# Kernel tuning notes

Measured on AMD Instinct MI355X. Metric: run time of the kernel, lower is better.

Reference implementation:

```python
import jax, jax.numpy as jnp
import numpy as np

B, L, D, NHEADS, P = 64, 256, 768, 8, 3
VOCAB, DEP, NLAYERS = 30522, 45, 2
LAM = 0.5


def _forward(src_mask, aspect_mask, lex, attention_mask,
             tok_emb, seg_emb, pool_w, pool_b, ln_a, ln_b,
             dep_emb, fc1_w, fc1_b, fc2_w, fc2_b,
             aq_w, aq_b, ak_w, ak_b, lq_w, lq_b, lk_w, lk_b, root_w,
             gcn_w, gcn_b, fc3_w, fc3_b, cls_w, cls_b, vlin_w,
             text_bert_indices, bert_segments_ids, ori_tag, head):
    b, l = text_bert_indices.shape
    d = tok_emb.shape[1]
    dk = d // NHEADS
    NEG = jnp.float32(-1e30)
    # stand-in BERT encoder: token + segment embeddings, tanh pooler on [CLS]
    seq = tok_emb[text_bert_indices] + seg_emb[bert_segments_ids]
    pooled = jnp.tanh(seq[:, 0] @ pool_w + pool_b)
    # torch LayerNorm variant: unbiased std (ddof=1)
    mean = seq.mean(-1, keepdims=True)
    std = jnp.std(seq, axis=-1, keepdims=True, ddof=1)
    gcn_in = ln_a * (seq - mean) / (std + 1e-6) + ln_b
    # in-place fmask[:,0]=1 mutates src_mask storage in torch -> effective mask
    sm = src_mask.at[:, 0].set(1.0)
    # dependency-tag score -> per-token softmax -> scatter into [L,L] adjacency
    dep_h = jax.nn.relu(dep_emb[ori_tag] @ fc1_w + fc1_b)
    dep_s = (dep_h @ fc2_w + fc2_b)[..., 0]                      # [B,L]
    dep_feat = jax.nn.softmax(dep_s * sm + (1.0 - sm) * NEG, axis=1)
    to_idx = jnp.arange(1, l)
    fro = head[:, :l - 1]                                        # [B,L-1]
    b_idx = jnp.arange(b)[:, None]
    vals = dep_feat[:, :l - 1]
    dep_adj = jnp.ones((b, l, l), jnp.float32)
    dep_adj = dep_adj.at[b_idx, fro, to_idx[None, :]].set(vals)
    dep_adj = dep_adj.at[b_idx, to_idx[None, :], fro].set(vals)
    # multi-head attention-as-adjacency (returns softmax weights only)
    q = (gcn_in @ aq_w + aq_b).reshape(b, l, NHEADS, dk).transpose(0, 2, 1, 3)
    k = (gcn_in @ ak_w + ak_b).reshape(b, l, NHEADS, dk).transpose(0, 2, 1, 3)
    scores = jnp.einsum('bhqd,bhkd->bhqk', q, k) / (jnp.sqrt(jnp.float32(dk)) + 1e-9)
    scores = jnp.where(sm[:, None, None, :] == 0, jnp.float32(-1e9), scores)
    adj_ag = jax.nn.softmax(scores, axis=-1).mean(axis=1)        # [B,L,L]
    eye = jnp.eye(l, dtype=jnp.float32)
    adj_ag = (adj_ag * (1.0 - eye) + eye) * sm[:, :, None]
    # structured latent attention (stand-in for missing StructuredAtt):
    # masked bilinear attention biased by dep_adj + root attention loss
    q2 = gcn_in @ lq_w + lq_b
    k2 = gcn_in @ lk_w + lk_b
    lat = jnp.einsum('bqd,bkd->bqk', q2, k2) / jnp.sqrt(jnp.float32(d))
    lat = lat + dep_adj + (1.0 - sm)[:, None, :] * (-10000.0)
    adj_latent = jax.nn.softmax(lat, axis=-1)
    root_p = jax.nn.softmax((gcn_in @ root_w)[..., 0] * sm + (1.0 - sm) * NEG, axis=1)
    loss_root = -jnp.mean(jnp.log(jnp.sum(root_p * aspect_mask, axis=1) + 1e-9))
    adj_latent = (adj_latent * (1.0 - eye) + eye) * sm[:, :, None]
    # gated dual-adjacency GCN layers
    H_l = gcn_in
    I_sem = gcn_in
    for layer in range(gcn_w.shape[0]):
        g_l = jax.nn.sigmoid(H_l)
        I_sem = (adj_ag @ H_l) @ gcn_w[layer] + gcn_b[layer]
        I_lat = (adj_latent @ H_l) @ gcn_w[layer] + gcn_b[layer]
        g = jax.nn.sigmoid(I_lat)
        lam_g = LAM * g
        I_com = (1.0 - lam_g) * I_sem + lam_g * I_lat
        H_out = jax.nn.relu(I_com @ fc3_w + fc3_b)
        H_l = g_l * H_out + (1.0 - g_l) * H_l
    # readout
    asp_wn = aspect_mask.sum(axis=1, keepdims=True)              # [B,1]
    m3 = sm[:, :, None]
    h_l = H_l * m3
    h_sem = I_sem * m3
    beta = jnp.einsum('bqd,bkd->bqk', h_l, h_sem) / 1000.0
    attn_o = jax.nn.softmax(beta.sum(axis=1, keepdims=True), axis=2)  # [B,1,L]
    outputs = (attn_o @ I_sem)[:, 0]                             # [B,D]
    sem_pool = (I_sem * aspect_mask[:, :, None]).sum(axis=1) / (asp_wn + 1e-9)
    final = jnp.concatenate([outputs, sem_pool, pooled], axis=-1)  # [B,3D]
    logits = final @ cls_w + cls_b
    e = (H_l @ vlin_w)[..., 0]
    lw = jax.nn.softmax(e, axis=1) * 50.0
    lw = lw * sm.at[:, 0].set(0.0)
    lexicon_loss = jnp.mean((lw - lex) ** 2)
    return logits, loss_root, lexicon_loss


def setup_inputs() -> dict:
    key = jax.random.key(0)
    ks = jax.random.split(key, 24)
    s = 0.02
    n = lambda i, shape: jax.random.normal(ks[i], shape, dtype=jnp.float32) * s
    inp = {}
    inp['text_bert_indices'] = jax.random.randint(ks[0], (B, L), 0, VOCAB, dtype=jnp.int32)
    inp['bert_segments_ids'] = jnp.zeros((B, L), jnp.int32)
    inp['attention_mask'] = jnp.ones((B, L), jnp.float32)
    inp['src_mask'] = jnp.ones((B, L), jnp.float32)
    inp['aspect_mask'] = jax.random.randint(ks[1], (B, L), 0, 2).astype(jnp.float32)
    inp['lex'] = jax.random.uniform(ks[2], (B, L), dtype=jnp.float32)
    inp['ori_tag'] = jax.random.randint(ks[3], (B, L), 0, DEP, dtype=jnp.int32)
    inp['head'] = jax.random.randint(ks[4], (B, L), 0, L, dtype=jnp.int32)
    inp['tok_emb'] = n(5, (VOCAB, D)); inp['seg_emb'] = n(6, (2, D))
    inp['pool_w'] = n(7, (D, D)); inp['pool_b'] = jnp.zeros((D,), jnp.float32)
    inp['ln_a'] = jnp.ones((D,), jnp.float32); inp['ln_b'] = jnp.zeros((D,), jnp.float32)
    inp['dep_emb'] = n(8, (DEP, 300))
    inp['fc1_w'] = n(9, (300, 256)); inp['fc1_b'] = jnp.zeros((256,), jnp.float32)
    inp['fc2_w'] = n(10, (256, 1)); inp['fc2_b'] = jnp.zeros((1,), jnp.float32)
    inp['aq_w'] = n(11, (D, D)); inp['aq_b'] = jnp.zeros((D,), jnp.float32)
    inp['ak_w'] = n(12, (D, D)); inp['ak_b'] = jnp.zeros((D,), jnp.float32)
    inp['lq_w'] = n(13, (D, D)); inp['lq_b'] = jnp.zeros((D,), jnp.float32)
    inp['lk_w'] = n(14, (D, D)); inp['lk_b'] = jnp.zeros((D,), jnp.float32)
    inp['root_w'] = n(15, (D, 1))
    inp['gcn_w'] = n(16, (NLAYERS, D, D)); inp['gcn_b'] = jnp.zeros((NLAYERS, D), jnp.float32)
    inp['fc3_w'] = n(17, (D, D)); inp['fc3_b'] = jnp.zeros((D,), jnp.float32)
    inp['cls_w'] = n(18, (3 * D, P)); inp['cls_b'] = jnp.zeros((P,), jnp.float32)
    inp['vlin_w'] = n(19, (D, 1))
    return inp


def reference(text_bert_indices, bert_segments_ids, attention_mask, src_mask, aspect_mask, lex,
              ori_tag, head, tok_emb, seg_emb, pool_w, pool_b, ln_a, ln_b, dep_emb,
              fc1_w, fc1_b, fc2_w, fc2_b, aq_w, aq_b, ak_w, ak_b, lq_w, lq_b, lk_w, lk_b,
              root_w, gcn_w, gcn_b, fc3_w, fc3_b, cls_w, cls_b, vlin_w):
    return _forward(src_mask, aspect_mask, lex, attention_mask,
                    tok_emb, seg_emb, pool_w, pool_b, ln_a, ln_b,
                    dep_emb, fc1_w, fc1_b, fc2_w, fc2_b,
                    aq_w, aq_b, ak_w, ak_b, lq_w, lq_b, lk_w, lk_b, root_w,
                    gcn_w, gcn_b, fc3_w, fc3_b, cls_w, cls_b, vlin_w,
                    text_bert_indices, bert_segments_ids, ori_tag, head)
```

## Files before the change

### kernel.cpp

```cpp
#include <hip/hip_runtime.h>
#include <hip/hip_bf16.h>
#include <math.h>

#define DI __device__ __forceinline__

constexpr int cB = 64, cL = 256, cD = 768;
constexpr long BLD = (long)cB * cL * cD;
constexpr long BLL = (long)cB * cL * cL;
constexpr long cLL = (long)cL * cL;
constexpr long cLD = (long)cL * cD;

typedef __attribute__((ext_vector_type(8))) short b8;
typedef __attribute__((ext_vector_type(4))) float f4;

#define GLDS(g, l)                                                    \
  __builtin_amdgcn_global_load_lds(                                   \
      (const __attribute__((address_space(1))) void*)(g),             \
      (__attribute__((address_space(3))) void*)(l), 16, 0, 0)

DI float wsum(float v) {
#pragma unroll
  for (int o = 32; o > 0; o >>= 1) v += __shfl_down(v, o, 64);
  return v;
}
DI float wsum_all(float v) {
#pragma unroll
  for (int m = 32; m > 0; m >>= 1) v += __shfl_xor(v, m, 64);
  return v;
}
DI float wmax_all(float v) {
#pragma unroll
  for (int m = 32; m > 0; m >>= 1) v = fmaxf(v, __shfl_xor(v, m, 64));
  return v;
}
DI float wmaxr(float v) {
#pragma unroll
  for (int o = 32; o > 0; o >>= 1) v = fmaxf(v, __shfl_down(v, o, 64));
  return v;
}
DI float blockSum(float v) {
  __shared__ float sh[4];
  v = wsum(v);
  __syncthreads();
  if ((threadIdx.x & 63) == 0) sh[threadIdx.x >> 6] = v;
  __syncthreads();
  return sh[0] + sh[1] + sh[2] + sh[3];
}
DI float blockMax(float v) {
  __shared__ float sh[4];
  v = wmaxr(v);
  __syncthreads();
  if ((threadIdx.x & 63) == 0) sh[threadIdx.x >> 6] = v;
  __syncthreads();
  return fmaxf(fmaxf(sh[0], sh[1]), fmaxf(sh[2], sh[3]));
}
DI float sigf(float x) { return 1.f / (1.f + expf(-x)); }

template <int OBF, int RELU, int BIAS, int EPI>
__global__ __launch_bounds__(256, 2) void bgemm(
    const __hip_bfloat16* __restrict__ A, const __hip_bfloat16* __restrict__ BT,
    void* __restrict__ Cv, const float* __restrict__ bias,
    float* __restrict__ auxf, __hip_bfloat16* __restrict__ auxb,
    int K, int lda, int ldb, int ldc,
    int zshift, int zmask, long sA1, long sA2, long sB1, long sB2, long sC,
    int czdiv) {
  __shared__ __hip_bfloat16 Asp[128 * 32];
  __shared__ __hip_bfloat16 Bsp[128 * 32];
  int z = blockIdx.z;
  A += (long)(z >> zshift) * sA1 + (long)(z & zmask) * sA2;
  BT += (long)(z >> zshift) * sB1 + (long)(z & zmask) * sB2;
  int tid = threadIdx.x;
  int lane = tid & 63, w = tid >> 6;
  int wr = w >> 1, wc = w & 1;
  int l16 = lane & 15, q = lane >> 4;
  int m0 = blockIdx.y << 7, n0 = blockIdx.x << 7;

  int fm = tid >> 2, fq = tid & 3;
  const __hip_bfloat16* Ap0 = A + (long)(m0 + fm) * lda + fq * 8;
  const __hip_bfloat16* Ap1 = A + (long)(m0 + fm + 64) * lda + fq * 8;
  const __hip_bfloat16* Bp0 = BT + (long)(n0 + fm) * ldb + fq * 8;
  const __hip_bfloat16* Bp1 = BT + (long)(n0 + fm + 64) * ldb + fq * 8;
  char* Aw0 = (char*)Asp + (w << 10);
  char* Aw1 = (char*)Asp + 4096 + (w << 10);
  char* Bw0 = (char*)Bsp + (w << 10);
  char* Bw1 = (char*)Bsp + 4096 + (w << 10);

  f4 acc[4][4];
#pragma unroll
  for (int i = 0; i < 4; i++)
#pragma unroll
    for (int j = 0; j < 4; j++) acc[i][j] = (f4){0.f, 0.f, 0.f, 0.f};

  for (int k0 = 0; k0 < K; k0 += 32) {
    GLDS(Ap0 + k0, Aw0);
    GLDS(Ap1 + k0, Aw1);
    GLDS(Bp0 + k0, Bw0);
    GLDS(Bp1 + k0, Bw1);
    __syncthreads();
    b8 af[4], bf[4];
#pragma unroll
    for (int i = 0; i < 4; i++)
      af[i] = *(const b8*)&Asp[(wr * 64 + i * 16 + l16) * 32 + q * 8];
#pragma unroll
    for (int j = 0; j < 4; j++)
      bf[j] = *(const b8*)&Bsp[(wc * 64 + j * 16 + l16) * 32 + q * 8];
#pragma unroll
    for (int i = 0; i < 4; i++)
#pragma unroll
      for (int j = 0; j < 4; j++)
        acc[i][j] = __builtin_amdgcn_mfma_f32_16x16x32_bf16(af[i], bf[j], acc[i][j], 0, 0, 0);
    __syncthreads();
  }
  if (EPI == 4) {
#pragma unroll
    for (int j = 0; j < 4; j++) {
      int n = n0 + wc * 64 + j * 16 + l16;
#pragma unroll
      for (int i = 0; i < 4; i++) {
        int m = m0 + wr * 64 + i * 16 + (q << 2);
        __hip_bfloat16 t4[4];
#pragma unroll
        for (int r = 0; r < 4; r++) t4[r] = __float2bfloat16(acc[i][j][r]);
        long bidx = (long)(m >> 8) * sC + (long)n * cL + (m & 255);
        *(uint2*)&((__hip_bfloat16*)Cv)[bidx] = *(uint2*)t4;
      }
    }
    return;
  }
  long cz = (long)(z >> czdiv) * sC;
#pragma unroll
  for (int j = 0; j < 4; j++) {
    int n = n0 + wc * 64 + j * 16 + l16;
    float bv = BIAS ? bias[n] : 0.f;
#pragma unroll
    for (int i = 0; i < 4; i++) {
#pragma unroll
      for (int r = 0; r < 4; r++) {
        int m = m0 + wr * 64 + i * 16 + q * 4 + r;
        long idx = cz + (long)m * ldc + n;
        float v = acc[i][j][r] + bv;
        if (EPI == 0) {
          if (RELU) v = fmaxf(v, 0.f);
          if (OBF)
            ((__hip_bfloat16*)Cv)[idx] = __float2bfloat16(v);
          else
            ((float*)Cv)[idx] = v;
        } else if (EPI == 3) {
          atomicAdd(&((float*)Cv)[idx], v);
        } else {
          v = fmaxf(v, 0.f);
          float h = auxf[idx];
          float g = sigf(h);
          float o = h + g * (v - h);
          auxf[idx] = o;
          auxb[idx] = __float2bfloat16(o);
        }
      }
    }
  }
}

__global__ __launch_bounds__(256, 2) void bgemm_dual(
    const __hip_bfloat16* __restrict__ A1g, const __hip_bfloat16* __restrict__ A2g,
    const __hip_bfloat16* __restrict__ BTg, float* __restrict__ IsemF,
    __hip_bfloat16* __restrict__ Icb, const float* __restrict__ bias,
    int write_isem) {
  __shared__ __hip_bfloat16 A1sp[128 * 32];
  __shared__ __hip_bfloat16 A2sp[128 * 32];
  __shared__ __hip_bfloat16 Bsp[128 * 32];
  int z = blockIdx.z;
  const __hip_bfloat16* A1 = A1g + (long)z * cLL;
  const __hip_bfloat16* A2 = A2g + (long)z * cLL;
  const __hip_bfloat16* BT = BTg + (long)z * cLD;
  int tid = threadIdx.x;
  int lane = tid & 63, w = tid >> 6;
  int wr = w >> 1, wc = w & 1;
  int l16 = lane & 15, q = lane >> 4;
  int m0 = blockIdx.y << 7, n0 = blockIdx.x << 7;

  int fm = tid >> 2, fq = tid & 3;
  const __hip_bfloat16* A1p0 = A1 + (long)(m0 + fm) * cL + fq * 8;
  const __hip_bfloat16* A1p1 = A1p0 + 64L * cL;
  const __hip_bfloat16* A2p0 = A2 + (long)(m0 + fm) * cL + fq * 8;
  const __hip_bfloat16* A2p1 = A2p0 + 64L * cL;
  const __hip_bfloat16* Bp0 = BT + (long)(n0 + fm) * cL + fq * 8;
  const __hip_bfloat16* Bp1 = Bp0 + 64L * cL;
  char* w10 = (char*)A1sp + (w << 10);
  char* w11 = (char*)A1sp + 4096 + (w << 10);
  char* w20 = (char*)A2sp + (w << 10);
  char* w21 = (char*)A2sp + 4096 + (w << 10);
  char* wb0 = (char*)Bsp + (w << 10);
  char* wb1 = (char*)Bsp + 4096 + (w << 10);

  f4 ac1[4][4], ac2[4][4];
#pragma unroll
  for (int i = 0; i < 4; i++)
#pragma unroll
    for (int j = 0; j < 4; j++) {
      ac1[i][j] = (f4){0.f, 0.f, 0.f, 0.f};
      ac2[i][j] = (f4){0.f, 0.f, 0.f, 0.f};
    }

  for (int k0 = 0; k0 < cL; k0 += 32) {
    GLDS(A1p0 + k0, w10);
    GLDS(A1p1 + k0, w11);
    GLDS(A2p0 + k0, w20);
    GLDS(A2p1 + k0, w21);
    GLDS(Bp0 + k0, wb0);
    GLDS(Bp1 + k0, wb1);
    __syncthreads();
    b8 a1f[4], a2f[4], bf[4];
#pragma unroll
    for (int i = 0; i < 4; i++) {
      a1f[i] = *(const b8*)&A1sp[(wr * 64 + i * 16 + l16) * 32 + q * 8];
      a2f[i] = *(const b8*)&A2sp[(wr * 64 + i * 16 + l16) * 32 + q * 8];
    }
#pragma unroll
    for (int j = 0; j < 4; j++)
      bf[j] = *(const b8*)&Bsp[(wc * 64 + j * 16 + l16) * 32 + q * 8];
#pragma unroll
    for (int i = 0; i < 4; i++)
#pragma unroll
      for (int j = 0; j < 4; j++) {
        ac1[i][j] = __builtin_amdgcn_mfma_f32_16x16x32_bf16(a1f[i], bf[j], ac1[i][j], 0, 0, 0);
        ac2[i][j] = __builtin_amdgcn_mfma_f32_16x16x32_bf16(a2f[i], bf[j], ac2[i][j], 0, 0, 0);
      }
    __syncthreads();
  }
  long cz = (long)z * cLD;
#pragma unroll
  for (int j = 0; j < 4; j++) {
    int n = n0 + wc * 64 + j * 16 + l16;
    float bv = bias[n];
#pragma unroll
    for (int i = 0; i < 4; i++) {
#pragma unroll
      for (int r = 0; r < 4; r++) {
        int m = m0 + wr * 64 + i * 16 + q * 4 + r;
        long idx = cz + (long)m * cD + n;
        float is = ac1[i][j][r] + bv;
        float il = ac2[i][j][r] + bv;
        float g = 0.5f * sigf(il);
        Icb[idx] = __float2bfloat16(is + g * (il - is));
        if (write_isem) IsemF[idx] = is;
      }
    }
  }
}

__global__ void k_wconv7(const float* __restrict__ s0, const float* __restrict__ s1,
                         const float* __restrict__ s2, const float* __restrict__ s3,
                         const float* __restrict__ s4, const float* __restrict__ s5,
                         const float* __restrict__ s6, __hip_bfloat16* __restrict__ dst) {
  const float* srcs[7] = {s0, s1, s2, s3, s4, s5, s6};
  const float* src = srcs[blockIdx.z];
  __hip_bfloat16* d = dst + (long)blockIdx.z * cD * cD;
  __shared__ float t[32][33];
  int k0 = blockIdx.x * 32, n0 = blockIdx.y * 32;
  int tx = threadIdx.x, ty = threadIdx.y;
#pragma unroll
  for (int i = 0; i < 32; i += 8) t[ty + i][tx] = src[(long)(k0 + ty + i) * cD + n0 + tx];
  __syncthreads();
#pragma unroll
  for (int i = 0; i < 32; i += 8)
    d[(long)(n0 + ty + i) * cD + k0 + tx] = __float2bfloat16(t[tx][ty + i]);
}

__global__ __launch_bounds__(256) void k_gcnin(
    const int* __restrict__ tbi, const int* __restrict__ bsi,
    const float* __restrict__ tok, const float* __restrict__ seg,
    const float* __restrict__ ln_a, const float* __restrict__ ln_b,
    const float* __restrict__ root_w,
    float* __restrict__ gcn_in, __hip_bfloat16* __restrict__ gib,
    float* __restrict__ x64, float* __restrict__ e1) {
  long bl = blockIdx.x;
  int t = tbi[bl], s = bsi[bl];
  const float* tr = tok + (long)t * cD;
  const float* sr = seg + (long)s * cD;
  float x[3];
  float ls = 0.f;
#pragma unroll
  for (int i = 0; i < 3; i++) {
    int d = threadIdx.x + (i << 8);
    x[i] = tr[d] + sr[d];
    ls += x[i];
  }
  if ((bl & 255) == 0) {
#pragma unroll
    for (int i = 0; i < 3; i++) x64[(bl >> 8) * cD + threadIdx.x + (i << 8)] = x[i];
  }
  float mean = blockSum(ls) * (1.f / 768.f);
  float lv = 0.f;
#pragma unroll
  for (int i = 0; i < 3; i++) { float c = x[i] - mean; lv += c * c; }
  float var = blockSum(lv) * (1.f / 767.f);
  float inv = 1.f / (sqrtf(var) + 1e-6f);
  float rdot = 0.f;
#pragma unroll
  for (int i = 0; i < 3; i++) {
    int d = threadIdx.x + (i << 8);
    float v = ln_a[d] * (x[i] - mean) * inv + ln_b[d];
    gcn_in[bl * cD + d] = v;
    gib[bl * cD + d] = __float2bfloat16(v);
    rdot += v * root_w[d];
  }
  float tot = blockSum(rdot);
  if (threadIdx.x == 0) e1[bl] = tot;
}

__global__ __launch_bounds__(256) void k_pool1(
    const float* __restrict__ x64, const float* __restrict__ pw,
    float* __restrict__ pacc) {
  __shared__ float pws[48][256];
  __shared__ float xs[16][48];
  int i0 = blockIdx.x * 48, j0 = blockIdx.y * 256, b0 = blockIdx.z * 16;
  for (int r = 0; r < 48; r++) pws[r][threadIdx.x] = pw[(long)(i0 + r) * cD + j0 + threadIdx.x];
  for (int idx = threadIdx.x; idx < 16 * 48; idx += 256)
    xs[idx / 48][idx % 48] = x64[(long)(b0 + idx / 48) * cD + i0 + idx % 48];
  __syncthreads();
  int j = threadIdx.x;
  for (int b = 0; b < 16; b++) {
    float acc = 0.f;
#pragma unroll 8
    for (int i = 0; i < 48; i++) acc += xs[b][i] * pws[i][j];
    atomicAdd(&pacc[(long)(b0 + b) * cD + j0 + j], acc);
  }
}
__global__ __launch_bounds__(256) void k_pool2(
    const float* __restrict__ pacc, const float* __restrict__ pb,
    float* __restrict__ pooled) {
  int b = blockIdx.x;
#pragma unroll
  for (int c = 0; c < 3; c++) {
    int j = (c << 8) + threadIdx.x;
    pooled[(long)b * cD + j] = tanhf(pacc[(long)b * cD + j] + pb[j]);
  }
}

__global__ __launch_bounds__(256) void k_s45(
    const float* __restrict__ dep_emb, const float* __restrict__ fc1w,
    const float* __restrict__ fc1b, const float* __restrict__ fc2w,
    const float* __restrict__ fc2b, float* __restrict__ s45) {
  int t = blockIdx.x;
  __shared__ float e[300];
  for (int i = threadIdx.x; i < 300; i += 256) e[i] = dep_emb[t * 300 + i];
  __syncthreads();
  int j = threadIdx.x;
  float h = fc1b[j];
  for (int i = 0; i < 300; i++) h += e[i] * fc1w[i * 256 + j];
  h = fmaxf(h, 0.f);
  float tot = blockSum(h * fc2w[j]);
  if (threadIdx.x == 0) s45[t] = tot + fc2b[0];
}

__global__ __launch_bounds__(256) void k_depfeat(
    const int* __restrict__ ori, const float* __restrict__ src_mask,
    const float* __restrict__ s45, float* __restrict__ dep_feat) {
  int b = blockIdx.x, l = threadIdx.x;
  float smv = (l == 0) ? 1.f : src_mask[b * cL + l];
  float sc = s45[ori[b * cL + l]] * smv + (1.f - smv) * (-1e30f);
  float mx = blockMax(sc);
  float ex = expf(sc - mx);
  float sum = blockSum(ex);
  dep_feat[b * cL + l] = ex / sum;
}

__global__ void k_bcat(const float* __restrict__ a, const float* __restrict__ b,
                       const float* __restrict__ c, const float* __restrict__ d,
                       float* __restrict__ o) {
  int i = blockIdx.x * 256 + threadIdx.x;
  float v = (i < 768) ? a[i] : (i < 1536) ? b[i - 768] : (i < 2304) ? c[i - 1536] : d[i - 2304];
  o[i] = v;
}

__global__ __launch_bounds__(256) void k_adjag_sm(
    const __hip_bfloat16* __restrict__ scores, const float* __restrict__ src_mask,
    __hip_bfloat16* __restrict__ adjag) {
  int b = blockIdx.x >> 8, i = blockIdx.x & 255;
  int tid = threadIdx.x, wave = tid >> 6, lane = tid & 63;
  __shared__ float accs[4][256];
  const float scale = 1.f / (sqrtf(96.f) + 1e-9f);
  float smj[4], acc[4];
#pragma unroll
  for (int c = 0; c < 4; c++) {
    int j = c * 64 + lane;
    smj[c] = (j == 0) ? 1.f : src_mask[b * cL + j];
    acc[c] = 0.f;
  }
  for (int hh = 0; hh < 2; hh++) {
    int h = wave * 2 + hh;
    const __hip_bfloat16* row = scores + (((long)(b * 8 + h)) * cL + i) * cL;
    float s[4], m = -1e30f;
#pragma unroll
    for (int c = 0; c < 4; c++) {
      s[c] = (smj[c] == 0.f) ? -1e9f : __bfloat162float(row[c * 64 + lane]) * scale;
      m = fmaxf(m, s[c]);
    }
    m = wmax_all(m);
    float es = 0.f;
#pragma unroll
    for (int c = 0; c < 4; c++) { s[c] = expf(s[c] - m); es += s[c]; }
    es = wsum_all(es);
    float inv = 1.f / es;
#pragma unroll
    for (int c = 0; c < 4; c++) acc[c] += s[c] * inv;
  }
#pragma unroll
  for (int c = 0; c < 4; c++) accs[wave][c * 64 + lane] = acc[c];
  __syncthreads();
  int j = tid;
  float tot = accs[0][j] + accs[1][j] + accs[2][j] + accs[3][j];
  float smi = (i == 0) ? 1.f : src_mask[b * cL + i];
  float v = (j == i) ? 1.f : tot * 0.125f;
  adjag[((long)b * cL + i) * cL + j] = __float2bfloat16(v * smi);
}

__global__ __launch_bounds__(256) void k_adjlat_sm(
    const float* __restrict__ latsc, const int* __restrict__ head,
    const float* __restrict__ df, const float* __restrict__ src_mask,
    __hip_bfloat16* __restrict__ adjlat) {
  int b = blockIdx.x >> 8, i = blockIdx.x & 255;
  int j = threadIdx.x;
  float smj = (j == 0) ? 1.f : src_mask[b * cL + j];
  float dep = 1.f;
  if (j >= 1 && head[b * cL + j - 1] == i) dep = df[b * cL + j - 1];
  if (i >= 1 && j == head[b * cL + i - 1]) dep = df[b * cL + i - 1];
  float s = latsc[((long)b * cL + i) * cL + j] * (1.f / sqrtf(768.f)) +
            dep + (1.f - smj) * (-10000.f);
  float mx = blockMax(s);
  float ex = expf(s - mx);
  float sum = blockSum(ex);
  float p = ex / sum;
  float smi = (i == 0) ? 1.f : src_mask[b * cL + i];
  adjlat[((long)b * cL + i) * cL + j] = __float2bfloat16(((j == i) ? 1.f : p) * smi);
}

__global__ __launch_bounds__(256) void k_rowdot(
    const float* __restrict__ X, const float* __restrict__ w, long wstride,
    float* __restrict__ e) {
  int r = blockIdx.x * 4 + (threadIdx.x >> 6);
  int lane = threadIdx.x & 63;
  const float4* row = (const float4*)(X + (long)r * cD);
  const float4* wp = (const float4*)(w + (long)(r >> 8) * wstride);
  float s = 0.f;
#pragma unroll
  for (int c = 0; c < 3; c++) {
    int idx = c * 64 + lane;
    float4 a = row[idx], b = wp[idx];
    s += a.x * b.x + a.y * b.y + a.z * b.z + a.w * b.w;
  }
  s = wsum(s);
  if (lane == 0) e[r] = s;
}

__global__ __launch_bounds__(256) void k_root2(
    const float* __restrict__ e1, const float* __restrict__ src_mask,
    const float* __restrict__ aspect_mask, float* __restrict__ out_loss) {
  int b = blockIdx.x, l = threadIdx.x;
  float r = e1[b * cL + l];
  float smv = (l == 0) ? 1.f : src_mask[b * cL + l];
  float sc = r * smv + (1.f - smv) * (-1e30f);
  float mx = blockMax(sc);
  float ex = expf(sc - mx);
  float sum = blockSum(ex);
  float p = ex / sum;
  float tot = blockSum(p * aspect_mask[b * cL + l]);
  if (l == 0) atomicAdd(out_loss, -logf(tot + 1e-9f) * (1.f / 64.f));
}

__global__ __launch_bounds__(256) void k_lex2(
    const float* __restrict__ e2, const float* __restrict__ src_mask,
    const float* __restrict__ lex, float* __restrict__ out_loss) {
  int b = blockIdx.x, l = threadIdx.x;
  float e = e2[b * cL + l];
  float mx = blockMax(e);
  float ex = expf(e - mx);
  float sum = blockSum(ex);
  float mult = (l == 0) ? 0.f : src_mask[b * cL + l];
  float lw = ex / sum * 50.f * mult;
  float d2 = lw - lex[b * cL + l];
  float tot = blockSum(d2 * d2);
  if (l == 0) atomicAdd(out_loss, tot * (1.f / (64.f * 256.f)));
}

__global__ __launch_bounds__(256) void k_hl(
    const float* __restrict__ H, const float* __restrict__ src_mask,
    float* __restrict__ hlsum) {
// ... 67 lines not shown
  const int* tbi = (const int*)d_in[0];
  const int* bsi = (const int*)d_in[1];
  const float* src_mask = (const float*)d_in[3];
  const float* aspect_mask = (const float*)d_in[4];
  const float* lex = (const float*)d_in[5];
  const int* ori = (const int*)d_in[6];
  const int* head = (const int*)d_in[7];
  const float* tok_emb = (const float*)d_in[8];
  const float* seg_emb = (const float*)d_in[9];
  const float* pool_w = (const float*)d_in[10];
  const float* pool_b = (const float*)d_in[11];
  const float* ln_a = (const float*)d_in[12];
  const float* ln_b = (const float*)d_in[13];
  const float* dep_emb = (const float*)d_in[14];
  const float* fc1_w = (const float*)d_in[15];
  const float* fc1_b = (const float*)d_in[16];
  const float* fc2_w = (const float*)d_in[17];
  const float* fc2_b = (const float*)d_in[18];
  const float* aq_w = (const float*)d_in[19];
  const float* aq_b = (const float*)d_in[20];
  const float* ak_w = (const float*)d_in[21];
  const float* ak_b = (const float*)d_in[22];
  const float* lq_w = (const float*)d_in[23];
  const float* lq_b = (const float*)d_in[24];
  const float* lk_w = (const float*)d_in[25];
  const float* lk_b = (const float*)d_in[26];
  const float* root_w = (const float*)d_in[27];
  const float* gcn_w = (const float*)d_in[28];
  const float* gcn_b = (const float*)d_in[29];
  const float* fc3_w = (const float*)d_in[30];
  const float* fc3_b = (const float*)d_in[31];
  const float* cls_w = (const float*)d_in[32];
  const float* cls_b = (const float*)d_in[33];
  const float* vlin_w = (const float*)d_in[34];

  float* out = (float*)d_out;
  float* ws = (float*)d_ws;
  float* gcnH = ws;
  float* Isem = gcnH + BLD;
  float* depfeat = Isem + BLD;
  float* s45 = depfeat + cB * cL;
  float* pooled = s45 + 64;
  float* x64 = pooled + cB * cD;
  float* hlsum = x64 + cB * cD;
  float* outputs = hlsum + cB * cD;
  float* sempool = outputs + cB * cD;
  float* pacc = sempool + cB * cD;
  float* e1 = pacc + cB * cD;
  float* e2 = e1 + cB * cL;
  float* sraw = e2 + cB * cL;
  float* wgt = sraw + cB * cL;
  float* asum = wgt + cB * cL;
  float* catb = asum + 64;
  float* latsc = Isem;
  __hip_bfloat16* gib = (__hip_bfloat16*)(catb + 3072);
  __hip_bfloat16* qkb = gib + BLD;
  __hip_bfloat16* scores = qkb + 4 * BLD;
  __hip_bfloat16* adjag_b = scores + 8 * BLL;
  __hip_bfloat16* adjlat_b = adjag_b + BLL;
  __hip_bfloat16* wbt = adjlat_b + BLL;
  __hip_bfloat16* HWbT = qkb + BLD;
  __hip_bfloat16* Icb = qkb + 2 * BLD;

  hipMemsetAsync((char*)d_out + 192 * sizeof(float), 0, 2 * sizeof(float), stream);
  hipMemsetAsync(hlsum, 0, 4 * cB * cD * sizeof(float), stream);
  hipMemsetAsync(latsc, 0, BLL * sizeof(float), stream);

  k_gcnin<<<cB * cL, 256, 0, stream>>>(tbi, bsi, tok_emb, seg_emb, ln_a, ln_b,
                                       root_w, gcnH, gib, x64, e1);
  k_s45<<<45, 256, 0, stream>>>(dep_emb, fc1_w, fc1_b, fc2_w, fc2_b, s45);
  k_depfeat<<<cB, 256, 0, stream>>>(ori, src_mask, s45, depfeat);
  k_pool1<<<dim3(16, 3, 4), 256, 0, stream>>>(x64, pool_w, pacc);
  k_pool2<<<cB, 256, 0, stream>>>(pacc, pool_b, pooled);
  k_bcat<<<12, 256, 0, stream>>>(aq_b, ak_b, lq_b, lk_b, catb);
  k_wconv7<<<dim3(24, 24, 7), dim3(32, 8), 0, stream>>>(
      aq_w, ak_w, lq_w, lk_w, gcn_w, gcn_w + (long)cD * cD, fc3_w, wbt);

  const long DD = (long)cD * cD;
  const long LD = cLD, LL = cLL;
  const long LP = (long)cL * 3072;

  bgemm<1, 0, 1, 0><<<dim3(24, 128, 1), 256, 0, stream>>>(
      gib, wbt, qkb, catb, nullptr, nullptr, cD, cD, cD, 3072,
      0, 0, 0, 0, 0, 0, 0, 0);

  bgemm<1, 0, 0, 0><<<dim3(2, 2, cB * 8), 256, 0, stream>>>(
      qkb, qkb + 768, scores, nullptr, nullptr, nullptr,
      96, 3072, 3072, cL, 3, 7, LP, 96, LP, 96, LL, 0);
  k_adjag_sm<<<cB * cL, 256, 0, stream>>>(scores, src_mask, adjag_b);

  bgemm<0, 0, 0, 3><<<dim3(2, 2, cB * 2), 256, 0, stream>>>(
      qkb + 1536, qkb + 2304, latsc, nullptr, nullptr, nullptr,
      384, 3072, 3072, cL, 1, 1, LP, 384, LP, 384, LL, 1);
  k_adjlat_sm<<<cB * cL, 256, 0, stream>>>(latsc, head, depfeat, src_mask, adjlat_b);

  k_root2<<<cB, 256, 0, stream>>>(e1, src_mask, aspect_mask, out + 192);

  for (int layer = 0; layer < 2; layer++) {
    const float* bb = gcn_b + (long)layer * cD;
    bgemm<1, 0, 0, 4><<<dim3(6, 128, 1), 256, 0, stream>>>(
        gib, wbt + (4 + layer) * DD, HWbT, nullptr, nullptr, nullptr,
        cD, cD, cD, cD, 0, 0, 0, 0, 0, 0, LD, 0);
    bgemm_dual<<<dim3(6, 2, cB), 256, 0, stream>>>(
        adjag_b, adjlat_b, HWbT, Isem, Icb, bb, layer == 1 ? 1 : 0);
    bgemm<0, 1, 1, 2><<<dim3(6, 128, 1), 256, 0, stream>>>(
        Icb, wbt + 6 * DD, nullptr, fc3_b, gcnH, gib,
        cD, cD, cD, cD, 0, 0, 0, 0, 0, 0, 0, 0);
  }

  k_hl<<<dim3(8, 3, cB), 256, 0, stream>>>(gcnH, src_mask, hlsum);
  k_rowdot<<<cB * cL / 4, 256, 0, stream>>>(Isem, hlsum, cD, sraw);
  k_attnw<<<cB, 256, 0, stream>>>(sraw, src_mask, aspect_mask, wgt, asum);
  k_wsum<<<dim3(8, 3, cB), 256, 0, stream>>>(Isem, wgt, aspect_mask, outputs, sempool);
  k_logits<<<cB, 256, 0, stream>>>(outputs, sempool, pooled, asum, cls_w, cls_b, out);
  k_rowdot<<<cB * cL / 4, 256, 0, stream>>>(gcnH, vlin_w, 0, e2);
  k_lex2<<<cB, 256, 0, stream>>>(e2, src_mask, lex, out + 193);
}
```

Before: 889.8 us.

## Double-buffer LDS tiles in bgemm and bgemm_dual to overlap loads with MFMA

Both GEMM kernels now keep two LDS buffers per operand. Each iteration issues the global-to-LDS loads for the next K tile before running MFMAs on the current one, and keeps a single barrier per iteration. The goal is to hide global load latency behind compute. The cost is double the LDS use, which may lower occupancy, and there is a correctness risk because global_load_lds completion is not explicitly waited on before the barrier.

```diff
diff --git a/kernel.cpp b/kernel.cpp
--- a/kernel.cpp
+++ b/kernel.cpp
@@ -64,8 +64,8 @@
     int K, int lda, int ldb, int ldc,
     int zshift, int zmask, long sA1, long sA2, long sB1, long sB2, long sC,
     int czdiv) {
-  __shared__ __hip_bfloat16 Asp[128 * 32];
-  __shared__ __hip_bfloat16 Bsp[128 * 32];
+  __shared__ __hip_bfloat16 Asp[2][128 * 32];
+  __shared__ __hip_bfloat16 Bsp[2][128 * 32];
   int z = blockIdx.z;
   A += (long)(z >> zshift) * sA1 + (long)(z & zmask) * sA2;
   BT += (long)(z >> zshift) * sB1 + (long)(z & zmask) * sB2;
@@ -91,25 +91,37 @@
 #pragma unroll
     for (int j = 0; j < 4; j++) acc[i][j] = (f4){0.f, 0.f, 0.f, 0.f};
 
+  GLDS(Ap0, Aw0);
+  GLDS(Ap1, Aw1);
+  GLDS(Bp0, Bw0);
+  GLDS(Bp1, Bw1);
+  __syncthreads();
+  int cur = 0;
   for (int k0 = 0; k0 < K; k0 += 32) {
-    GLDS(Ap0 + k0, Aw0);
-    GLDS(Ap1 + k0, Aw1);
-    GLDS(Bp0 + k0, Bw0);
-    GLDS(Bp1 + k0, Bw1);
-    __syncthreads();
+    int k1 = k0 + 32;
+    if (k1 < K) {
+      int nb = (cur ^ 1) * 8192;
+      GLDS(Ap0 + k1, Aw0 + nb);
+      GLDS(Ap1 + k1, Aw1 + nb);
+      GLDS(Bp0 + k1, Bw0 + nb);
+      GLDS(Bp1 + k1, Bw1 + nb);
+    }
+    const __hip_bfloat16* As = Asp[cur];
+    const __hip_bfloat16* Bs = Bsp[cur];
     b8 af[4], bf[4];
 #pragma unroll
     for (int i = 0; i < 4; i++)
-      af[i] = *(const b8*)&Asp[(wr * 64 + i * 16 + l16) * 32 + q * 8];
+      af[i] = *(const b8*)&As[(wr * 64 + i * 16 + l16) * 32 + q * 8];
 #pragma unroll
     for (int j = 0; j < 4; j++)
-      bf[j] = *(const b8*)&Bsp[(wc * 64 + j * 16 + l16) * 32 + q * 8];
+      bf[j] = *(const b8*)&Bs[(wc * 64 + j * 16 + l16) * 32 + q * 8];
 #pragma unroll
     for (int i = 0; i < 4; i++)
 #pragma unroll
       for (int j = 0; j < 4; j++)
         acc[i][j] = __builtin_amdgcn_mfma_f32_16x16x32_bf16(af[i], bf[j], acc[i][j], 0, 0, 0);
     __syncthreads();
+    cur ^= 1;
   }
   if (EPI == 4) {
 #pragma unroll
@@ -165,9 +177,9 @@
     const __hip_bfloat16* __restrict__ BTg, float* __restrict__ IsemF,
     __hip_bfloat16* __restrict__ Icb, const float* __restrict__ bias,
     int write_isem) {
-  __shared__ __hip_bfloat16 A1sp[128 * 32];
-  __shared__ __hip_bfloat16 A2sp[128 * 32];
-  __shared__ __hip_bfloat16 Bsp[128 * 32];
+  __shared__ __hip_bfloat16 A1sp[2][128 * 32];
+  __shared__ __hip_bfloat16 A2sp[2][128 * 32];
+  __shared__ __hip_bfloat16 Bsp[2][128 * 32];
   int z = blockIdx.z;
   const __hip_bfloat16* A1 = A1g + (long)z * cLL;
   const __hip_bfloat16* A2 = A2g + (long)z * cLL;
@@ -201,23 +213,37 @@
       ac2[i][j] = (f4){0.f, 0.f, 0.f, 0.f};
     }
 
+  GLDS(A1p0, w10);
+  GLDS(A1p1, w11);
+  GLDS(A2p0, w20);
+  GLDS(A2p1, w21);
+  GLDS(Bp0, wb0);
+  GLDS(Bp1, wb1);
+  __syncthreads();
+  int cur = 0;
   for (int k0 = 0; k0 < cL; k0 += 32) {
-    GLDS(A1p0 + k0, w10);
-    GLDS(A1p1 + k0, w11);
-    GLDS(A2p0 + k0, w20);
-    GLDS(A2p1 + k0, w21);
-    GLDS(Bp0 + k0, wb0);
-    GLDS(Bp1 + k0, wb1);
-    __syncthreads();
+    int k1 = k0 + 32;
+    if (k1 < cL) {
+      int nb = (cur ^ 1) * 8192;
+      GLDS(A1p0 + k1, w10 + nb);
+      GLDS(A1p1 + k1, w11 + nb);
+      GLDS(A2p0 + k1, w20 + nb);
+      GLDS(A2p1 + k1, w21 + nb);
+      GLDS(Bp0 + k1, wb0 + nb);
+      GLDS(Bp1 + k1, wb1 + nb);
+    }
+    const __hip_bfloat16* A1s = A1sp[cur];
+    const __hip_bfloat16* A2s = A2sp[cur];
+    const __hip_bfloat16* Bs = Bsp[cur];
     b8 a1f[4], a2f[4], bf[4];
 #pragma unroll
     for (int i = 0; i < 4; i++) {
-      a1f[i] = *(const b8*)&A1sp[(wr * 64 + i * 16 + l16) * 32 + q * 8];
-      a2f[i] = *(const b8*)&A2sp[(wr * 64 + i * 16 + l16) * 32 + q * 8];
+      a1f[i] = *(const b8*)&A1s[(wr * 64 + i * 16 + l16) * 32 + q * 8];
+      a2f[i] = *(const b8*)&A2s[(wr * 64 + i * 16 + l16) * 32 + q * 8];
     }
 #pragma unroll
     for (int j = 0; j < 4; j++)
-      bf[j] = *(const b8*)&Bsp[(wc * 64 + j * 16 + l16) * 32 + q * 8];
+      bf[j] = *(const b8*)&Bs[(wc * 64 + j * 16 + l16) * 32 + q * 8];
 #pragma unroll
     for (int i = 0; i < 4; i++)
 #pragma unroll
@@ -226,6 +252,7 @@
         ac2[i][j] = __builtin_amdgcn_mfma_f32_16x16x32_bf16(a2f[i], bf[j], ac2[i][j], 0, 0, 0);
       }
     __syncthreads();
+    cur ^= 1;
   }
   long cz = (long)z * cLD;
 #pragma unroll
```

After: 906.6 us. No clear change (+1.9%).

## Add 256x256-tile 8-wave pipelined GEMM for the fused QK projection

Applied to the files above, without the earlier changes.

Replaces the generic 128x128 bgemm used for the fused Q/K/latent projection (16384x3072x768) with a dedicated 256x256 tile kernel using 512 threads, swizzled LDS, direct global-to-LDS loads and double buffering with explicit waitcnt, barriers and sched_barrier. The larger tile is meant to improve operand reuse and overlap loads with MFMA work. In exchange it uses 128KB of LDS per block, which limits occupancy, and launches only 768 blocks; the two-blocks-per-CU launch bound may not be reachable.

```diff
diff --git a/kernel.cpp b/kernel.cpp
--- a/kernel.cpp
+++ b/kernel.cpp
@@ -17,6 +17,16 @@
   __builtin_amdgcn_global_load_lds(                                   \
       (const __attribute__((address_space(1))) void*)(g),             \
       (__attribute__((address_space(3))) void*)(l), 16, 0, 0)
+
+#define SCB __builtin_amdgcn_sched_barrier(0)
+#define BAR()                        \
+  {                                  \
+    SCB;                             \
+    __builtin_amdgcn_s_barrier();    \
+    SCB;                             \
+  }
+#define VMC4 asm volatile("s_waitcnt vmcnt(4)" ::: "memory")
+#define VMC0 asm volatile("s_waitcnt vmcnt(0)" ::: "memory")
 
 DI float wsum(float v) {
 #pragma unroll
@@ -55,6 +65,144 @@
   return fmaxf(fmaxf(sh[0], sh[1]), fmaxf(sh[2], sh[3]));
 }
 DI float sigf(float x) { return 1.f / (1.f + expf(-x)); }
+
+__global__ __launch_bounds__(512, 2) void bgemm256(
+    const __hip_bfloat16* __restrict__ A, const __hip_bfloat16* __restrict__ BT,
+    __hip_bfloat16* __restrict__ C, const float* __restrict__ bias) {
+  constexpr int K = 768, LDA = 768, LDB = 768, LDC = 3072, NT = K / 64;
+  __shared__ __hip_bfloat16 lds[65536];
+  char* ldsA = (char*)lds;
+  char* ldsB = (char*)lds + 65536;
+  const int tid = threadIdx.x;
+  const int lane = tid & 63, w = tid >> 6;
+  const int wm = w >> 2, wn = w & 3;
+  const int l16 = lane & 15, q4 = lane >> 4;
+  const int m0 = blockIdx.y << 8, n0 = blockIdx.x << 8;
+
+  int goffA[2], goffB[2];
+  char* stA[2];
+  char* stB[2];
+#pragma unroll
+  for (int u = 0; u < 2; u++) {
+    int ci = u * 512 + tid;
+    int P = ci * 16;
+    int Lb = P ^ (((P >> 7) & 7) << 4);
+    int rowL = Lb >> 6, c16 = (Lb >> 4) & 3;
+    goffA[u] = (m0 + rowL) * LDA + c16 * 8;
+    goffB[u] = (n0 + rowL) * LDB + c16 * 8;
+    stA[u] = ldsA + u * 8192 + (w << 10);
+    stB[u] = ldsB + u * 8192 + (w << 10);
+  }
+  const int swzr = ((l16 >> 1) & 7) << 4;
+  const int aoff = (((wm * 128 + l16) * 64) + q4 * 16) ^ swzr;
+  const int boff = (((wn * 64 + l16) * 64) + q4 * 16) ^ swzr;
+
+  f4 acc[8][4];
+#pragma unroll
+  for (int i = 0; i < 8; i++)
+#pragma unroll
+    for (int j = 0; j < 4; j++) acc[i][j] = (f4){0.f, 0.f, 0.f, 0.f};
+
+#define STG(Gp, go, sd, bufo, kb)              \
+  {                                            \
+    GLDS(Gp + go[0] + (kb), sd[0] + (bufo));   \
+    GLDS(Gp + go[1] + (kb), sd[1] + (bufo));   \
+  }
+
+  STG(A, goffA, stA, 0, 0);
+  STG(BT, goffB, stB, 0, 0);
+  STG(A, goffA, stA, 16384, 32);
+  STG(BT, goffB, stB, 16384, 32);
+  VMC4;
+  BAR();
+
+  for (int t = 0; t < NT; ++t) {
+    const int p = t & 1;
+    const char* Ab = ldsA + p * 32768;
+    const char* Bb = ldsB + p * 32768;
+    const int qo = (p ^ 1) * 32768;
+    const bool st = (t + 1 < NT);
+    const int kn = (t + 1) * 64;
+    b8 a[8], b0, b1;
+#pragma unroll
+    for (int i = 0; i < 8; i++) a[i] = *(const b8*)(Ab + aoff + i * 1024);
+    b0 = *(const b8*)(Bb + boff);
+    b1 = *(const b8*)(Bb + boff + 1024);
+    if (st) STG(A, goffA, stA, qo, kn);
+    BAR();
+    __builtin_amdgcn_s_setprio(1);
+#pragma unroll
+    for (int i = 0; i < 8; i++) {
+      acc[i][0] = __builtin_amdgcn_mfma_f32_16x16x32_bf16(a[i], b0, acc[i][0], 0, 0, 0);
+      acc[i][1] = __builtin_amdgcn_mfma_f32_16x16x32_bf16(a[i], b1, acc[i][1], 0, 0, 0);
+    }
+    __builtin_amdgcn_s_setprio(0);
+    BAR();
+    b0 = *(const b8*)(Bb + boff + 2048);
+    b1 = *(const b8*)(Bb + boff + 3072);
+    if (st) {
+      STG(BT, goffB, stB, qo, kn);
+      VMC4;
+    } else {
+      VMC0;
+    }
+    BAR();
+    __builtin_amdgcn_s_setprio(1);
+#pragma unroll
+    for (int i = 0; i < 8; i++) {
+      acc[i][2] = __builtin_amdgcn_mfma_f32_16x16x32_bf16(a[i], b0, acc[i][2], 0, 0, 0);
+      acc[i][3] = __builtin_amdgcn_mfma_f32_16x16x32_bf16(a[i], b1, acc[i][3], 0, 0, 0);
+    }
+    __builtin_amdgcn_s_setprio(0);
+    BAR();
+#pragma unroll
+    for (int i = 0; i < 8; i++) a[i] = *(const b8*)(Ab + 16384 + aoff + i * 1024);
+    b0 = *(const b8*)(Bb + 16384 + boff);
+    b1 = *(const b8*)(Bb + 16384 + boff + 1024);
+    if (st) STG(A, goffA, stA, qo + 16384, kn + 32);
+    BAR();
+    __builtin_amdgcn_s_setprio(1);
+#pragma unroll
+    for (int i = 0; i < 8; i++) {
+      acc[i][0] = __builtin_amdgcn_mfma_f32_16x16x32_bf16(a[i], b0, acc[i][0], 0, 0, 0);
+      acc[i][1] = __builtin_amdgcn_mfma_f32_16x16x32_bf16(a[i], b1, acc[i][1], 0, 0, 0);
+    }
+    __builtin_amdgcn_s_setprio(0);
+    BAR();
+    b0 = *(const b8*)(Bb + 16384 + boff + 2048);
+    b1 = *(const b8*)(Bb + 16384 + boff + 3072);
+    if (st) {
+      STG(BT, goffB, stB, qo + 16384, kn + 32);
+      VMC4;
+    } else {
+      VMC0;
+    }
+    BAR();
+    __builtin_amdgcn_s_setprio(1);
+#pragma unroll
+    for (int i = 0; i < 8; i++) {
+      acc[i][2] = __builtin_amdgcn_mfma_f32_16x16x32_bf16(a[i], b0, acc[i][2], 0, 0, 0);
+      acc[i][3] = __builtin_amdgcn_mfma_f32_16x16x32_bf16(a[i], b1, acc[i][3], 0, 0, 0);
+    }
+    __builtin_amdgcn_s_setprio(0);
+    BAR();
+  }
+#undef STG
+
+#pragma unroll
+  for (int j = 0; j < 4; j++) {
+    int n = n0 + wn * 64 + j * 16 + l16;
+    float bv = bias[n];
+#pragma unroll
+    for (int i = 0; i < 8; i++) {
+#pragma unroll
+      for (int r = 0; r < 4; r++) {
+        int m = m0 + wm * 128 + i * 16 + q4 * 4 + r;
+        C[(long)m * LDC + n] = __float2bfloat16(acc[i][j][r] + bv);
+      }
+    }
+  }
+}
 
 template <int OBF, int RELU, int BIAS, int EPI>
 __global__ __launch_bounds__(256, 2) void bgemm(
@@ -634,9 +782,7 @@
   const long LD = cLD, LL = cLL;
   const long LP = (long)cL * 3072;
 
-  bgemm<1, 0, 1, 0><<<dim3(24, 128, 1), 256, 0, stream>>>(
-      gib, wbt, qkb, catb, nullptr, nullptr, cD, cD, cD, 3072,
-      0, 0, 0, 0, 0, 0, 0, 0);
+  bgemm256<<<dim3(12, 64), 512, 0, stream>>>(gib, wbt, qkb, catb);
 
   bgemm<1, 0, 0, 0><<<dim3(2, 2, cB * 8), 256, 0, stream>>>(
       qkb, qkb + 768, scores, nullptr, nullptr, nullptr,
```

Result: no change. 903.9 us (+1.6%).

## Fuse QK score GEMMs with softmax into flash-style adjacency kernels

Applied to the files above, without the earlier changes.

Replaces the per-head score GEMM plus separate softmax kernels, and the split-K latent score GEMM with atomics, with a single templated kernel. It computes QK^T tiles with MFMA, applies masking, the dependency bias and softmax in registers, and writes the bf16 adjacency directly. This removes the materialised bf16 score tensor, the fp32 latent score buffer and its memset. The GCN input LayerNorm now uses one wave per row and drops the fp32 gcn_in write. The highway epilogue reads its state from the bf16 copy and writes fp32 only on the last layer, trading some precision for less memory traffic.

```diff
diff --git a/kernel.cpp b/kernel.cpp
--- a/kernel.cpp
+++ b/kernel.cpp
@@ -145,15 +145,13 @@
             ((__hip_bfloat16*)Cv)[idx] = __float2bfloat16(v);
           else
             ((float*)Cv)[idx] = v;
-        } else if (EPI == 3) {
-          atomicAdd(&((float*)Cv)[idx], v);
         } else {
           v = fmaxf(v, 0.f);
-          float h = auxf[idx];
+          float h = __bfloat162float(auxb[idx]);
           float g = sigf(h);
           float o = h + g * (v - h);
-          auxf[idx] = o;
           auxb[idx] = __float2bfloat16(o);
+          if (auxf) auxf[idx] = o;
         }
       }
     }
@@ -248,6 +246,174 @@
   }
 }
 
+template <int NH>
+__global__ __launch_bounds__(256, 2) void k_qkadj(
+    const __hip_bfloat16* __restrict__ qkb, const float* __restrict__ src_mask,
+    const int* __restrict__ headv, const float* __restrict__ df,
+    __hip_bfloat16* __restrict__ outA) {
+  constexpr int KH = (NH == 8) ? 96 : 768;
+  constexpr int QOFF = (NH == 8) ? 0 : 1536;
+  constexpr int KOFF = (NH == 8) ? 768 : 2304;
+  const float scale = (NH == 8) ? (1.f / (sqrtf(96.f) + 1e-9f)) : (1.f / sqrtf(768.f));
+  __shared__ __hip_bfloat16 Qs[64 * 32];
+  __shared__ __hip_bfloat16 Ks[256 * 32];
+  __shared__ float red[4][64];
+  const int b = blockIdx.y, m0 = blockIdx.x << 6;
+  const int tid = threadIdx.x, lane = tid & 63, w = tid >> 6;
+  const int l16 = lane & 15, q = lane >> 4;
+  const long rowbase = (long)b * cL;
+  const __hip_bfloat16* Qg = qkb + (rowbase + m0 + (tid >> 2)) * 3072 + (tid & 3) * 8 + QOFF;
+  const __hip_bfloat16* Kg = qkb + (rowbase + (tid >> 2)) * 3072 + (tid & 3) * 8 + KOFF;
+  char* qdst = (char*)Qs + (w << 10);
+
+  float smj[4];
+  int hcol[4];
+  float dfc[4];
+#pragma unroll
+  for (int j = 0; j < 4; j++) {
+    int col = w * 64 + j * 16 + l16;
+    smj[j] = (col == 0) ? 1.f : src_mask[b * cL + col];
+    if (NH == 1) {
+      hcol[j] = (col >= 1) ? headv[b * cL + col - 1] : -1;
+      dfc[j] = (col >= 1) ? df[b * cL + col - 1] : 0.f;
+    }
+  }
+  float smi_[4][4];
+  int hrow_[4][4];
+  float dfr_[4][4];
+#pragma unroll
+  for (int i = 0; i < 4; i++)
+#pragma unroll
+    for (int r = 0; r < 4; r++) {
+      int grow = m0 + i * 16 + q * 4 + r;
+      smi_[i][r] = (grow == 0) ? 1.f : src_mask[b * cL + grow];
+      if (NH == 1) {
+        hrow_[i][r] = (grow >= 1) ? headv[b * cL + grow - 1] : -1;
+        dfr_[i][r] = (grow >= 1) ? df[b * cL + grow - 1] : 0.f;
+      }
+    }
+
+  f4 aag[4][4];
+#pragma unroll
+  for (int i = 0; i < 4; i++)
+#pragma unroll
+    for (int j = 0; j < 4; j++) aag[i][j] = (f4){0.f, 0.f, 0.f, 0.f};
+
+  f4 sa[4][4];
+  float inv_[4][4];
+  for (int h = 0; h < NH; h++) {
+    const int hk = h * 96;
+#pragma unroll
+    for (int i = 0; i < 4; i++)
+#pragma unroll
+      for (int j = 0; j < 4; j++) sa[i][j] = (f4){0.f, 0.f, 0.f, 0.f};
+    for (int k0 = 0; k0 < KH; k0 += 32) {
+      __syncthreads();
+      GLDS(Qg + hk + k0, qdst);
+#pragma unroll
+      for (int u = 0; u < 4; u++)
+        GLDS(Kg + (long)u * 196608 + hk + k0, (char*)Ks + u * 4096 + (w << 10));
+      __syncthreads();
+      b8 af[4], bf[4];
+#pragma unroll
+      for (int i = 0; i < 4; i++)
+        af[i] = *(const b8*)&Qs[(i * 16 + l16) * 32 + q * 8];
+#pragma unroll
+      for (int j = 0; j < 4; j++)
+        bf[j] = *(const b8*)&Ks[(w * 64 + j * 16 + l16) * 32 + q * 8];
+#pragma unroll
+      for (int i = 0; i < 4; i++)
+#pragma unroll
+        for (int j = 0; j < 4; j++)
+          sa[i][j] = __builtin_amdgcn_mfma_f32_16x16x32_bf16(af[i], bf[j], sa[i][j], 0, 0, 0);
+    }
+#pragma unroll
+    for (int i = 0; i < 4; i++)
+#pragma unroll
+      for (int j = 0; j < 4; j++)
+#pragma unroll
+        for (int r = 0; r < 4; r++) {
+          float raw = sa[i][j][r];
+          float v;
+          if (NH == 1) {
+            int grow = m0 + i * 16 + q * 4 + r;
+            int col = w * 64 + j * 16 + l16;
+            float dep = 1.f;
+            if (hcol[j] == grow) dep = dfc[j];
+            if (col == hrow_[i][r]) dep = dfr_[i][r];
+            v = raw * scale + dep + (1.f - smj[j]) * -10000.f;
+          } else {
+            v = (smj[j] == 0.f) ? -1e9f : raw * scale;
+          }
+          sa[i][j][r] = v;
+        }
+    float rm_[4][4];
+#pragma unroll
+    for (int i = 0; i < 4; i++)
+#pragma unroll
+      for (int r = 0; r < 4; r++) {
+        float m = fmaxf(fmaxf(sa[i][0][r], sa[i][1][r]), fmaxf(sa[i][2][r], sa[i][3][r]));
+#pragma unroll
+        for (int o = 1; o < 16; o <<= 1) m = fmaxf(m, __shfl_xor(m, o, 64));
+        if (l16 == 0) red[w][i * 16 + q * 4 + r] = m;
+        rm_[i][r] = m;
+      }
+    __syncthreads();
+#pragma unroll
+    for (int i = 0; i < 4; i++)
+#pragma unroll
+      for (int r = 0; r < 4; r++) {
+        int lr = i * 16 + q * 4 + r;
+        rm_[i][r] = fmaxf(fmaxf(red[0][lr], red[1][lr]), fmaxf(red[2][lr], red[3][lr]));
+      }
+    __syncthreads();
+#pragma unroll
+    for (int i = 0; i < 4; i++)
+#pragma unroll
+      for (int r = 0; r < 4; r++) {
+        float s0 = 0.f;
+#pragma unroll
+        for (int j = 0; j < 4; j++) {
+          float e = expf(sa[i][j][r] - rm_[i][r]);
+          sa[i][j][r] = e;
+          s0 += e;
+        }
+#pragma unroll
+        for (int o = 1; o < 16; o <<= 1) s0 += __shfl_xor(s0, o, 64);
+        if (l16 == 0) red[w][i * 16 + q * 4 + r] = s0;
+      }
+    __syncthreads();
+#pragma unroll
+    for (int i = 0; i < 4; i++)
+#pragma unroll
+      for (int r = 0; r < 4; r++) {
+        int lr = i * 16 + q * 4 + r;
+        inv_[i][r] = 1.f / (red[0][lr] + red[1][lr] + red[2][lr] + red[3][lr]);
+      }
+    if (NH == 8) {
+#pragma unroll
+      for (int i = 0; i < 4; i++)
+#pragma unroll
+        for (int j = 0; j < 4; j++)
+#pragma unroll
+          for (int r = 0; r < 4; r++) aag[i][j][r] += sa[i][j][r] * inv_[i][r];
+    }
+  }
+#pragma unroll
+  for (int j = 0; j < 4; j++) {
+    int col = w * 64 + j * 16 + l16;
+#pragma unroll
+    for (int i = 0; i < 4; i++)
+#pragma unroll
+      for (int r = 0; r < 4; r++) {
+        int grow = m0 + i * 16 + q * 4 + r;
+        float p = (NH == 8) ? aag[i][j][r] * 0.125f : sa[i][j][r] * inv_[i][r];
+        float v = (col == grow) ? 1.f : p;
+        outA[((long)b * cL + grow) * cL + col] = __float2bfloat16(v * smi_[i][r]);
+      }
+  }
+}
+
 __global__ void k_wconv7(const float* __restrict__ s0, const float* __restrict__ s1,
                          const float* __restrict__ s2, const float* __restrict__ s3,
                          const float* __restrict__ s4, const float* __restrict__ s5,
@@ -270,42 +436,41 @@
     const int* __restrict__ tbi, const int* __restrict__ bsi,
     const float* __restrict__ tok, const float* __restrict__ seg,
     const float* __restrict__ ln_a, const float* __restrict__ ln_b,
-    const float* __restrict__ root_w,
-    float* __restrict__ gcn_in, __hip_bfloat16* __restrict__ gib,
+    const float* __restrict__ root_w, __hip_bfloat16* __restrict__ gib,
     float* __restrict__ x64, float* __restrict__ e1) {
-  long bl = blockIdx.x;
+  int wave = threadIdx.x >> 6, lane = threadIdx.x & 63;
+  long bl = (long)blockIdx.x * 4 + wave;
   int t = tbi[bl], s = bsi[bl];
   const float* tr = tok + (long)t * cD;
   const float* sr = seg + (long)s * cD;
-  float x[3];
+  float x[12];
   float ls = 0.f;
 #pragma unroll
-  for (int i = 0; i < 3; i++) {
-    int d = threadIdx.x + (i << 8);
-    x[i] = tr[d] + sr[d];
-    ls += x[i];
+  for (int c = 0; c < 12; c++) {
+    int d = lane + (c << 6);
+    x[c] = tr[d] + sr[d];
+    ls += x[c];
   }
   if ((bl & 255) == 0) {
 #pragma unroll
-    for (int i = 0; i < 3; i++) x64[(bl >> 8) * cD + threadIdx.x + (i << 8)] = x[i];
-  }
-  float mean = blockSum(ls) * (1.f / 768.f);
+    for (int c = 0; c < 12; c++) x64[(bl >> 8) * cD + lane + (c << 6)] = x[c];
+  }
+  float mean = wsum_all(ls) * (1.f / 768.f);
   float lv = 0.f;
 #pragma unroll
-  for (int i = 0; i < 3; i++) { float c = x[i] - mean; lv += c * c; }
-  float var = blockSum(lv) * (1.f / 767.f);
+  for (int c = 0; c < 12; c++) { float d2 = x[c] - mean; lv += d2 * d2; }
+  float var = wsum_all(lv) * (1.f / 767.f);
   float inv = 1.f / (sqrtf(var) + 1e-6f);
   float rdot = 0.f;
 #pragma unroll
-  for (int i = 0; i < 3; i++) {
-    int d = threadIdx.x + (i << 8);
-    float v = ln_a[d] * (x[i] - mean) * inv + ln_b[d];
-    gcn_in[bl * cD + d] = v;
+  for (int c = 0; c < 12; c++) {
+    int d = lane + (c << 6);
+    float v = ln_a[d] * (x[c] - mean) * inv + ln_b[d];
     gib[bl * cD + d] = __float2bfloat16(v);
     rdot += v * root_w[d];
   }
-  float tot = blockSum(rdot);
-  if (threadIdx.x == 0) e1[bl] = tot;
+  float tot = wsum_all(rdot);
+  if (lane == 0) e1[bl] = tot;
 }
 
 __global__ __launch_bounds__(256) void k_pool1(
@@ -371,68 +536,6 @@
   int i = blockIdx.x * 256 + threadIdx.x;
   float v = (i < 768) ? a[i] : (i < 1536) ? b[i - 768] : (i < 2304) ? c[i - 1536] : d[i - 2304];
   o[i] = v;
-}
-
-__global__ __launch_bounds__(256) void k_adjag_sm(
-    const __hip_bfloat16* __restrict__ scores, const float* __restrict__ src_mask,
-    __hip_bfloat16* __restrict__ adjag) {
-  int b = blockIdx.x >> 8, i = blockIdx.x & 255;
-  int tid = threadIdx.x, wave = tid >> 6, lane = tid & 63;
-  __shared__ float accs[4][256];
-  const float scale = 1.f / (sqrtf(96.f) + 1e-9f);
-  float smj[4], acc[4];
-#pragma unroll
-  for (int c = 0; c < 4; c++) {
-    int j = c * 64 + lane;
-    smj[c] = (j == 0) ? 1.f : src_mask[b * cL + j];
-    acc[c] = 0.f;
-  }
-  for (int hh = 0; hh < 2; hh++) {
-    int h = wave * 2 + hh;
-    const __hip_bfloat16* row = scores + (((long)(b * 8 + h)) * cL + i) * cL;
-    float s[4], m = -1e30f;
-#pragma unroll
-    for (int c = 0; c < 4; c++) {
-      s[c] = (smj[c] == 0.f) ? -1e9f : __bfloat162float(row[c * 64 + lane]) * scale;
-      m = fmaxf(m, s[c]);
-    }
-    m = wmax_all(m);
-    float es = 0.f;
-#pragma unroll
-    for (int c = 0; c < 4; c++) { s[c] = expf(s[c] - m); es += s[c]; }
-    es = wsum_all(es);
-    float inv = 1.f / es;
-#pragma unroll
-    for (int c = 0; c < 4; c++) acc[c] += s[c] * inv;
-  }
-#pragma unroll
-  for (int c = 0; c < 4; c++) accs[wave][c * 64 + lane] = acc[c];
-  __syncthreads();
-  int j = tid;
-  float tot = accs[0][j] + accs[1][j] + accs[2][j] + accs[3][j];
-  float smi = (i == 0) ? 1.f : src_mask[b * cL + i];
-  float v = (j == i) ? 1.f : tot * 0.125f;
-  adjag[((long)b * cL + i) * cL + j] = __float2bfloat16(v * smi);
-}
-
-__global__ __launch_bounds__(256) void k_adjlat_sm(
-    const float* __restrict__ latsc, const int* __restrict__ head,
-    const float* __restrict__ df, const float* __restrict__ src_mask,
-    __hip_bfloat16* __restrict__ adjlat) {
-  int b = blockIdx.x >> 8, i = blockIdx.x & 255;
-  int j = threadIdx.x;
-  float smj = (j == 0) ? 1.f : src_mask[b * cL + j];
-  float dep = 1.f;
-  if (j >= 1 && head[b * cL + j - 1] == i) dep = df[b * cL + j - 1];
-  if (i >= 1 && j == head[b * cL + i - 1]) dep = df[b * cL + i - 1];
-  float s = latsc[((long)b * cL + i) * cL + j] * (1.f / sqrtf(768.f)) +
-            dep + (1.f - smj) * (-10000.f);
-  float mx = blockMax(s);
-  float ex = expf(s - mx);
-  float sum = blockSum(ex);
-  float p = ex / sum;
-  float smi = (i == 0) ? 1.f : src_mask[b * cL + i];
-  adjlat[((long)b * cL + i) * cL + j] = __float2bfloat16(((j == i) ? 1.f : p) * smi);
 }
 
 __global__ __launch_bounds__(256) void k_rowdot(
@@ -606,7 +709,6 @@
   float* wgt = sraw + cB * cL;
   float* asum = wgt + cB * cL;
   float* catb = asum + 64;
-  float* latsc = Isem;
   __hip_bfloat16* gib = (__hip_bfloat16*)(catb + 3072);
   __hip_bfloat16* qkb = gib + BLD;
   __hip_bfloat16* scores = qkb + 4 * BLD;
@@ -618,10 +720,9 @@
 
   hipMemsetAsync((char*)d_out + 192 * sizeof(float), 0, 2 * sizeof(float), stream);
   hipMemsetAsync(hlsum, 0, 4 * cB * cD * sizeof(float), stream);
-  hipMemsetAsync(latsc, 0, BLL * sizeof(float), stream);
-
-  k_gcnin<<<cB * cL, 256, 0, stream>>>(tbi, bsi, tok_emb, seg_emb, ln_a, ln_b,
-                                       root_w, gcnH, gib, x64, e1);
+
+  k_gcnin<<<cB * cL / 4, 256, 0, stream>>>(tbi, bsi, tok_emb, seg_emb, ln_a, ln_b,
+                                           root_w, gib, x64, e1);
   k_s45<<<45, 256, 0, stream>>>(dep_emb, fc1_w, fc1_b, fc2_w, fc2_b, s45);
   k_depfeat<<<cB, 256, 0, stream>>>(ori, src_mask, s45, depfeat);
   k_pool1<<<dim3(16, 3, 4), 256, 0, stream>>>(x64, pool_w, pacc);
@@ -631,22 +732,14 @@
       aq_w, ak_w, lq_w, lk_w, gcn_w, gcn_w + (long)cD * cD, fc3_w, wbt);
 
   const long DD = (long)cD * cD;
-  const long LD = cLD, LL = cLL;
-  const long LP = (long)cL * 3072;
+  const long LD = cLD;
 
   bgemm<1, 0, 1, 0><<<dim3(24, 128, 1), 256, 0, stream>>>(
       gib, wbt, qkb, catb, nullptr, nullptr, cD, cD, cD, 3072,
       0, 0, 0, 0, 0, 0, 0, 0);
 
-  bgemm<1, 0, 0, 0><<<dim3(2, 2, cB * 8), 256, 0, stream>>>(
-      qkb, qkb + 768, scores, nullptr, nullptr, nullptr,
-      96, 3072, 3072, cL, 3, 7, LP, 96, LP, 96, LL, 0);
-  k_adjag_sm<<<cB * cL, 256, 0, stream>>>(scores, src_mask, adjag_b);
-
-  bgemm<0, 0, 0, 3><<<dim3(2, 2, cB * 2), 256, 0, stream>>>(
-      qkb + 1536, qkb + 2304, latsc, nullptr, nullptr, nullptr,
-      384, 3072, 3072, cL, 1, 1, LP, 384, LP, 384, LL, 1);
-  k_adjlat_sm<<<cB * cL, 256, 0, stream>>>(latsc, head, depfeat, src_mask, adjlat_b);
+  k_qkadj<8><<<dim3(4, cB), 256, 0, stream>>>(qkb, src_mask, nullptr, nullptr, adjag_b);
+  k_qkadj<1><<<dim3(4, cB), 256, 0, stream>>>(qkb, src_mask, head, depfeat, adjlat_b);
 
   k_root2<<<cB, 256, 0, stream>>>(e1, src_mask, aspect_mask, out + 192);
 
@@ -658,7 +751,7 @@
     bgemm_dual<<<dim3(6, 2, cB), 256, 0, stream>>>(
         adjag_b, adjlat_b, HWbT, Isem, Icb, bb, layer == 1 ? 1 : 0);
     bgemm<0, 1, 1, 2><<<dim3(6, 128, 1), 256, 0, stream>>>(
-        Icb, wbt + 6 * DD, nullptr, fc3_b, gcnH, gib,
+        Icb, wbt + 6 * DD, nullptr, fc3_b, layer == 1 ? gcnH : nullptr, gib,
         cD, cD, cD, cD, 0, 0, 0, 0, 0, 0, 0, 0);
   }
 
```

Result: faster. 807.0 us (-9.3%).
